# Kernel optimization log

Measured on AMD Instinct MI355X. Metric: run time of the kernel, lower is better.

The kernel has to match this reference:

```python
import jax, jax.numpy as jnp
import numpy as np

# Bit-slice widths from SliceMethod([1,2,4]) on both input and weight sides
# (MSB-first, 7 magnitude bits total, sign carried per-element in each slice).
IN_SLICES = (1, 2, 4)
W_SLICES = (1, 2, 4)


def _l2norm(a):
    # F.normalize(a, p=2, dim=1)
    n = jnp.sqrt(jnp.sum(a * a, axis=1, keepdims=True))
    return a / jnp.maximum(n, 1e-12)


def _quantize(a, nbits):
    # symmetric fixed-point quantization to `nbits` magnitude bits,
    # dynamic per-tensor scale (bw_e=None -> fixed-point path)
    Q = float(2 ** nbits - 1)
    scale = jnp.max(jnp.abs(a))
    q = jnp.round(a / scale * Q)  # integer-valued float32 in [-Q, Q]
    return q, scale / Q


def _bit_slices(q, widths):
    # split |q| into bit groups (MSB-first per slice_method order); sign is
    # folded into each slice so recombination sum_k 2^off_k * slice_k == q
    sign = jnp.sign(q)
    mag = jnp.abs(q)
    total = sum(widths)
    slices = []
    off = total
    for w in widths:
        off -= w
        s = jnp.mod(jnp.floor(mag / (2.0 ** off)), 2.0 ** w)
        slices.append((sign * s, off))
    return slices


def setup_inputs() -> dict:
    key = jax.random.key(0)
    kx, kw = jax.random.split(key)
    x = jax.random.normal(kx, (4096, 1024), dtype=jnp.float32)
    weight = jax.random.normal(kw, (8192, 1024), dtype=jnp.float32)  # vectors.t -> [M, D]
    return {"x": x, "weight": weight}


def reference(x, weight):
    xn = _l2norm(x)        # [B, D]
    wn = _l2norm(weight)   # [M, D]
    qx, sx = _quantize(xn, sum(IN_SLICES))
    qw, sw = _quantize(wn, sum(W_SLICES))
    x_slices = _bit_slices(qx, IN_SLICES)
    w_slices = _bit_slices(qw, W_SLICES)
    # map_reduce_dot_func: 9 slice-pair low-bit GEMMs, recombined with 2^(oi+oj)
    acc = jnp.zeros((x.shape[0], weight.shape[0]), dtype=jnp.float32)
    for xs_k, ox in x_slices:
        for ws_k, ow in w_slices:
            acc = acc + (2.0 ** (ox + ow)) * jnp.einsum('bd,md->bm', xs_k, ws_k)
    cos = acc * sx * sw  # dequantize -> cosine similarity in [-1, 1]
    return 1.0 - cos
```

## Files before the change

kernel.cpp:

```cpp
#include <hip/hip_runtime.h>
#include <cstdint>
#include <cstddef>


#define D_COLS 1024
#define M_ROWS 4096
#define N_ROWS 8192

using i32x4 = __attribute__((ext_vector_type(4))) int;

__device__ __forceinline__ void gload_lds16(const void* g, void* lds) {
  __builtin_amdgcn_global_load_lds(
      (const __attribute__((address_space(1))) uint32_t*)g,
      (__attribute__((address_space(3))) uint32_t*)lds, 16, 0, 0);
}

__global__ __launch_bounds__(256) void rownorm_kernel(
    const float* __restrict__ x, const float* __restrict__ w,
    float* __restrict__ invnorm, float* __restrict__ rmax) {
  const int row = blockIdx.x;
  const float* a = (row < M_ROWS) ? x + (size_t)row * D_COLS
                                  : w + (size_t)(row - M_ROWS) * D_COLS;
  const float4 v = ((const float4*)a)[threadIdx.x];
  float ss = v.x * v.x + v.y * v.y + v.z * v.z + v.w * v.w;
  float mx = fmaxf(fmaxf(fabsf(v.x), fabsf(v.y)), fmaxf(fabsf(v.z), fabsf(v.w)));
#pragma unroll
  for (int off = 32; off; off >>= 1) {
    ss += __shfl_down(ss, off, 64);
    mx = fmaxf(mx, __shfl_down(mx, off, 64));
  }
  __shared__ float s_ss[4], s_mx[4];
  const int wave = threadIdx.x >> 6, lane = threadIdx.x & 63;
  if (lane == 0) { s_ss[wave] = ss; s_mx[wave] = mx; }
  __syncthreads();
  if (threadIdx.x == 0) {
    float tss = (s_ss[0] + s_ss[1]) + (s_ss[2] + s_ss[3]);
    float tmx = fmaxf(fmaxf(s_mx[0], s_mx[1]), fmaxf(s_mx[2], s_mx[3]));
    float inv = 1.0f / fmaxf(sqrtf(tss), 1e-12f);
    invnorm[row] = inv;
    rmax[row] = tmx * inv;
  }
}

__global__ __launch_bounds__(1024) void scale_reduce_kernel(
    const float* __restrict__ rmax, float* __restrict__ scales) {
  const int t = threadIdx.x;
  float mx = 0.f, mw = 0.f;
  for (int i = t; i < M_ROWS; i += 1024) mx = fmaxf(mx, rmax[i]);
  for (int i = t; i < N_ROWS; i += 1024) mw = fmaxf(mw, rmax[M_ROWS + i]);
#pragma unroll
  for (int off = 32; off; off >>= 1) {
    mx = fmaxf(mx, __shfl_down(mx, off, 64));
    mw = fmaxf(mw, __shfl_down(mw, off, 64));
  }
  __shared__ float smx[16], smw[16];
  const int wave = t >> 6, lane = t & 63;
  if (lane == 0) { smx[wave] = mx; smw[wave] = mw; }
  __syncthreads();
  if (t == 0) {
    float a = 0.f, b = 0.f;
#pragma unroll
    for (int i = 0; i < 16; ++i) { a = fmaxf(a, smx[i]); b = fmaxf(b, smw[i]); }
    scales[0] = a;
    scales[1] = b;
  }
}

__global__ __launch_bounds__(256) void quant_fused_kernel(
    const float* __restrict__ x, const float* __restrict__ w,
    const float* __restrict__ invnorm, const float* __restrict__ scales,
    uint4* __restrict__ qx, uint4* __restrict__ qw) {
  __shared__ uint4 T[128][16];
  const int b = blockIdx.x;
  const float* a;
  const float* inv;
  float sc;
  uint4* img;
  int bb;
  if (b < 128) { a = x; inv = invnorm; sc = scales[0]; img = qx; bb = b; }
  else { a = w; inv = invnorm + M_ROWS; sc = scales[1]; img = qw; bb = b - 128; }
  const int t = threadIdx.x;
  const int g = bb & 3;
  const int Q = bb >> 2;
  const float s = 127.0f / sc;

  const int cc_l = t & 15;
  const int tr = t >> 4;
#pragma unroll
  for (int rc = 0; rc < 8; ++rc) {
    const int rl = rc * 16 + tr;
    const int r = Q * 128 + rl;
    const float f = inv[r] * s;
    const float4* src = (const float4*)(a + (size_t)r * D_COLS + (g * 16 + cc_l) * 16);
    unsigned pk[4];
#pragma unroll
    for (int q = 0; q < 4; ++q) {
      const float4 v = src[q];
      const int q0 = (int)rintf(v.x * f), q1 = (int)rintf(v.y * f);
      const int q2 = (int)rintf(v.z * f), q3 = (int)rintf(v.w * f);
      pk[q] = (unsigned)(q0 & 0xff) | ((unsigned)(q1 & 0xff) << 8) |
              ((unsigned)(q2 & 0xff) << 16) | ((unsigned)(q3 & 0xff) << 24);
    }
    T[rl][cc_l ^ (rl & 15)] = make_uint4(pk[0], pk[1], pk[2], pk[3]);
  }
  __syncthreads();

  const int cc_w = g * 16 + (t >> 4);
  const int rw = t & 15;
  uint4* dst = img + (size_t)(Q * 16 + (cc_w >> 2)) * 512 + (cc_w & 3) * 128;
#pragma unroll
  for (int i = 0; i < 8; ++i) {
    const int rl = i * 16 + rw;
    dst[rl] = T[rl][(t >> 4) ^ (rl & 15)];
  }
}

__global__ __launch_bounds__(256, 2) void gemm_i8_kernel(
    const char* __restrict__ qx, const char* __restrict__ qw,
    const float* __restrict__ sx, const float* __restrict__ sw,
    float* __restrict__ out) {
  __shared__ __align__(16) char L[49152];
  const int t = threadIdx.x;
  const int wave = t >> 6, lane = t & 63;
  const int wr = wave >> 1, wc = wave & 1;
  const int rl = lane & 15, ko = lane >> 4;

  const int fid = blockIdx.x;
  const int swz = (fid & 7) * 128 + (fid >> 3);
  const int bx = swz & 63;
  const int by = swz >> 6;

  const char* sa0 = qx + (size_t)(2 * by) * 16 * 8192;
  const char* sa1 = qx + (size_t)(2 * by + 1) * 16 * 8192;
  const char* sb0 = qw + (size_t)bx * 16 * 8192;

  i32x4 acc[8][4] = {};

#define ISSUE_HT(ks)                                                          \
  {                                                                           \
    const size_t so_ = (size_t)(ks) * 8192;                                   \
    char* d_ = L + ((ks) & 1) * 24576;                                        \
    gload_lds16(sa0 + so_ + wave * 2048 + lane * 16, d_ + wave * 2048);       \
    gload_lds16(sa0 + so_ + wave * 2048 + 1024 + lane * 16,                   \
                d_ + wave * 2048 + 1024);                                     \
    gload_lds16(sa1 + so_ + wave * 2048 + lane * 16, d_ + 8192 + wave * 2048);\
    gload_lds16(sa1 + so_ + wave * 2048 + 1024 + lane * 16,                   \
                d_ + 8192 + wave * 2048 + 1024);                              \
    gload_lds16(sb0 + so_ + wave * 2048 + lane * 16, d_ + 16384 + wave * 2048);\
    gload_lds16(sb0 + so_ + wave * 2048 + 1024 + lane * 16,                   \
                d_ + 16384 + wave * 2048 + 1024);                             \
  }

#define STEP(ks, VM)                                                          \
  {                                                                           \
    if ((ks) + 1 < 16) ISSUE_HT((ks) + 1);                                    \
    asm volatile("s_waitcnt vmcnt(" #VM ")" ::: "memory");                    \
    asm volatile("s_barrier" ::: "memory");                                   \
    const char* Ab_ = L + ((ks) & 1) * 24576 + wr * 8192;                     \
    const char* Bb_ = L + ((ks) & 1) * 24576 + 16384;                         \
    i32x4 af_[8], bf_[4];                                                     \
    _Pragma("unroll") for (int m_ = 0; m_ < 8; ++m_)                          \
      af_[m_] = *(const i32x4*)(Ab_ + (ko * 128 + m_ * 16 + rl) * 16);        \
    _Pragma("unroll") for (int n_ = 0; n_ < 4; ++n_)                          \
      bf_[n_] = *(const i32x4*)(Bb_ +                                         \
          (ko * 128 + wc * 64 + n_ * 16 + rl) * 16);                          \
    __builtin_amdgcn_s_setprio(1);                                            \
    _Pragma("unroll") for (int m_ = 0; m_ < 8; ++m_)                          \
      _Pragma("unroll") for (int n_ = 0; n_ < 4; ++n_)                        \
        acc[m_][n_] = __builtin_amdgcn_mfma_i32_16x16x64_i8(                  \
            af_[m_], bf_[n_], acc[m_][n_], 0, 0, 0);                          \
    __builtin_amdgcn_s_setprio(0);                                            \
    asm volatile("s_barrier" ::: "memory");                                   \
  }

  ISSUE_HT(0);

#pragma unroll 1
  for (int ks = 0; ks < 15; ++ks) STEP(ks, 6);
  STEP(15, 0);
#undef STEP
#undef ISSUE_HT

  const float cs = sx[0] * sw[0] * (1.0f / 16129.0f);
  const int rowBase = by * 256 + wr * 128;
  const int colBase = bx * 128 + wc * 64;
#pragma unroll
  for (int m = 0; m < 8; ++m) {
    const int row = rowBase + m * 16 + ko * 4;
#pragma unroll
    for (int n = 0; n < 4; ++n) {
      const int col = colBase + n * 16 + rl;
#pragma unroll
      for (int j = 0; j < 4; ++j)
        out[(size_t)(row + j) * N_ROWS + col] = 1.0f - (float)acc[m][n][j] * cs;
    }
  }
}

extern "C" void kernel_launch(void* const* d_in, const int* in_sizes, int n_in,
                              void* d_out, int out_size, void* d_ws, size_t ws_size,
                              hipStream_t stream) {
  const float* x = (const float*)d_in[0];
  const float* w = (const float*)d_in[1];
  float* out = (float*)d_out;

  char* ws = (char*)d_ws;
  char* qx = ws;
  char* qw = ws + (size_t)M_ROWS * D_COLS;
  float* invnorm = (float*)(ws + (size_t)(M_ROWS + N_ROWS) * D_COLS);
  float* rmax = invnorm + (M_ROWS + N_ROWS);
  float* scales = rmax + (M_ROWS + N_ROWS);

  rownorm_kernel<<<M_ROWS + N_ROWS, 256, 0, stream>>>(x, w, invnorm, rmax);
  scale_reduce_kernel<<<1, 1024, 0, stream>>>(rmax, scales);

  quant_fused_kernel<<<384, 256, 0, stream>>>(
      x, w, invnorm, scales, (uint4*)qx, (uint4*)qw);

  gemm_i8_kernel<<<dim3(1024), 256, 0, stream>>>(qx, qw, &scales[0], &scales[1], out);
}
```

Before: 74.51 us.

## Triple-buffer LDS in int8 GEMM to prefetch two K-steps ahead

Grows the GEMM's LDS staging from two buffers to three rotating buffers and issues global-to-LDS loads two K-steps ahead instead of one. Each iteration now waits for its own tile, uses a single barrier, then starts the next prefetch into the buffer freed in the previous step. The intent is to hide more global load latency and drop one barrier per K-step. In exchange, LDS per block rises to 72 KB, which may limit how many blocks fit per CU alongside the requested two-block occupancy.

```diff
diff --git a/kernel.cpp b/kernel.cpp
--- a/kernel.cpp
+++ b/kernel.cpp
@@ -119,7 +119,7 @@
     const char* __restrict__ qx, const char* __restrict__ qw,
     const float* __restrict__ sx, const float* __restrict__ sw,
     float* __restrict__ out) {
-  __shared__ __align__(16) char L[49152];
+  __shared__ __align__(16) char L[73728];
   const int t = threadIdx.x;
   const int wave = t >> 6, lane = t & 63;
   const int wr = wave >> 1, wc = wave & 1;
@@ -136,10 +136,10 @@
 
   i32x4 acc[8][4] = {};
 
-#define ISSUE_HT(ks)                                                          \
+#define ISSUE_HT(ks, bufoff)                                                  \
   {                                                                           \
     const size_t so_ = (size_t)(ks) * 8192;                                   \
-    char* d_ = L + ((ks) & 1) * 24576;                                        \
+    char* d_ = L + (bufoff);                                                  \
     gload_lds16(sa0 + so_ + wave * 2048 + lane * 16, d_ + wave * 2048);       \
     gload_lds16(sa0 + so_ + wave * 2048 + 1024 + lane * 16,                   \
                 d_ + wave * 2048 + 1024);                                     \
@@ -151,13 +151,10 @@
                 d_ + 16384 + wave * 2048 + 1024);                             \
   }
 
-#define STEP(ks, VM)                                                          \
+#define COMPUTE(curoff)                                                       \
   {                                                                           \
-    if ((ks) + 1 < 16) ISSUE_HT((ks) + 1);                                    \
-    asm volatile("s_waitcnt vmcnt(" #VM ")" ::: "memory");                    \
-    asm volatile("s_barrier" ::: "memory");                                   \
-    const char* Ab_ = L + ((ks) & 1) * 24576 + wr * 8192;                     \
-    const char* Bb_ = L + ((ks) & 1) * 24576 + 16384;                         \
+    const char* Ab_ = L + (curoff) + wr * 8192;                               \
+    const char* Bb_ = L + (curoff) + 16384;                                   \
     i32x4 af_[8], bf_[4];                                                     \
     _Pragma("unroll") for (int m_ = 0; m_ < 8; ++m_)                          \
       af_[m_] = *(const i32x4*)(Ab_ + (ko * 128 + m_ * 16 + rl) * 16);        \
@@ -170,15 +167,25 @@
         acc[m_][n_] = __builtin_amdgcn_mfma_i32_16x16x64_i8(                  \
             af_[m_], bf_[n_], acc[m_][n_], 0, 0, 0);                          \
     __builtin_amdgcn_s_setprio(0);                                            \
-    asm volatile("s_barrier" ::: "memory");                                   \
-  }
-
-  ISSUE_HT(0);
-
+  }
+
+  ISSUE_HT(0, 0);
+  ISSUE_HT(1, 24576);
+
+  int cur = 0, stg = 49152;
 #pragma unroll 1
-  for (int ks = 0; ks < 15; ++ks) STEP(ks, 6);
-  STEP(15, 0);
-#undef STEP
+  for (int ks = 0; ks < 15; ++ks) {
+    asm volatile("s_waitcnt vmcnt(6)" ::: "memory");
+    asm volatile("s_barrier" ::: "memory");
+    if (ks + 2 < 16) ISSUE_HT(ks + 2, stg);
+    COMPUTE(cur);
+    cur += 24576; if (cur == 73728) cur = 0;
+    stg += 24576; if (stg == 73728) stg = 0;
+  }
+  asm volatile("s_waitcnt vmcnt(0)" ::: "memory");
+  asm volatile("s_barrier" ::: "memory");
+  COMPUTE(cur);
+#undef COMPUTE
 #undef ISSUE_HT
 
   const float cs = sx[0] * sw[0] * (1.0f / 16129.0f);
```

After: 73.16 us. About the same (-1.8%).
